# Performance work log

Hardware: AMD Instinct MI355X
Metric: run time of the kernel (lower is better)

## Reference

```python
import jax, jax.numpy as jnp
import numpy as np

B, S, H = 2, 1024, 2048
NH, NKV, HD = 16, 8, 128
GROUPS = NH // NKV
THETA = 1000000.0
SPARSITY = 0.4  # q_len > 512 -> vision_sparse_attention_sparsity_ratio
TOP_K = max(1, min(S, int(SPARSITY * S)))


def _rope(q, k, position_ids):
    # inv_freq: [HD/2]
    inv_freq = 1.0 / (THETA ** (jnp.arange(0, HD, 2, dtype=jnp.float32) / HD))
    freqs = position_ids.astype(jnp.float32)[:, :, None] * inv_freq  # [B,S,HD/2]
    emb = jnp.concatenate([freqs, freqs], axis=-1)                   # [B,S,HD]
    cos = jnp.cos(emb)[:, None].astype(q.dtype)  # [B,1,S,HD] (unsqueeze_dim=1)
    sin = jnp.sin(emb)[:, None].astype(q.dtype)
    rot = lambda x: jnp.concatenate([-x[..., HD // 2:], x[..., :HD // 2]], axis=-1)
    return q * cos + rot(q) * sin, k * cos + rot(k) * sin


def setup_inputs() -> dict:
    key = jax.random.key(0)
    ks = jax.random.split(key, 10)
    sc = 0.02
    inp = {
        'hidden_states': jax.random.normal(ks[0], (B, S, H), jnp.float32),
        'wq': jax.random.normal(ks[1], (NH * HD, H), jnp.float32) * sc,
        'bq': jax.random.normal(ks[2], (NH * HD,), jnp.float32) * sc,
        'wk': jax.random.normal(ks[3], (NKV * HD, H), jnp.float32) * sc,
        'bk': jax.random.normal(ks[4], (NKV * HD,), jnp.float32) * sc,
        'wv': jax.random.normal(ks[5], (NKV * HD, H), jnp.float32) * sc,
        'bv': jax.random.normal(ks[6], (NKV * HD,), jnp.float32) * sc,
        'wo': jax.random.normal(ks[7], (H, NH * HD), jnp.float32) * sc,
        'bo': jax.random.normal(ks[8], (H,), jnp.float32) * sc,
        'position_ids': jnp.tile(jnp.arange(S, dtype=jnp.int32)[None, :], (B, 1)),
    }
    return inp


def reference(hidden_states, wq, bq, wk, bk, wv, bv, wo, bo, position_ids):
    # QKV projections -> [B, heads, S, HD]
    q = (hidden_states @ wq.T + bq).reshape(B, S, NH, HD).transpose(0, 2, 1, 3)
    k = (hidden_states @ wk.T + bk).reshape(B, S, NKV, HD).transpose(0, 2, 1, 3)
    v = (hidden_states @ wv.T + bv).reshape(B, S, NKV, HD).transpose(0, 2, 1, 3)

    q, k = _rope(q, k, position_ids)

    # GQA: repeat_interleave KV heads along head axis
    k = jnp.repeat(k, GROUPS, axis=1)
    v = jnp.repeat(v, GROUPS, axis=1)

    scores = jnp.einsum('bhqd,bhkd->bhqk', q, k) / jnp.sqrt(jnp.float32(HD))

    # VectorizedSparseAttention: keep top-k weights per query, -inf elsewhere
    topk_vals = jax.lax.top_k(scores, TOP_K)[0]          # sorted descending
    thresh = topk_vals[..., -1:]                         # k-th largest per row
    sparse = jnp.where(scores >= thresh, scores, -jnp.inf)

    probs = jax.nn.softmax(sparse.astype(jnp.float32), axis=-1).astype(q.dtype)
    attn = jnp.einsum('bhqk,bhkd->bhqd', probs, v)       # [B,NH,S,HD]
    attn = attn.transpose(0, 2, 1, 3).reshape(B, S, NH * HD)
    return attn @ wo.T + bo
```

## Files before the change

kernel.cpp:

```cpp
#include <hip/hip_runtime.h>
#include <hip/hip_bf16.h>

constexpr int B_ = 2, S_ = 1024, H_ = 2048;
constexpr int NH_ = 16, NKV_ = 8, HD_ = 128, GROUPS_ = 2;
constexpr int TOPK_ = 409;
constexpr int QSTRIDE = NH_ * HD_;
constexpr int KSTRIDE = NKV_ * HD_;
constexpr int QB_ = 16;

typedef __attribute__((ext_vector_type(8))) short short8;
typedef __attribute__((ext_vector_type(4))) float f32x4;
typedef __attribute__((ext_vector_type(4))) unsigned u32x4;
typedef __attribute__((ext_vector_type(4))) unsigned short ush4;

__device__ inline unsigned fkey(float x) {
  unsigned u = __float_as_uint(x);
  return (u & 0x80000000u) ? ~u : (u | 0x80000000u);
}
__device__ inline unsigned short bf16_rne(float x) {
  unsigned u = __float_as_uint(x);
  unsigned r = u + 0x7FFFu + ((u >> 16) & 1u);
  return (unsigned short)(r >> 16);
}
__device__ inline float bf16_to_f(unsigned short h) {
  return __uint_as_float((unsigned)h << 16);
}
__device__ inline unsigned packsplit(float x) {
  unsigned u = __float_as_uint(x);
  unsigned r = (u + 0x7FFFu + ((u >> 16) & 1u)) & 0xFFFF0000u;
  float rem = x - __uint_as_float(r);
  unsigned v = __float_as_uint(rem);
  unsigned l = (v + 0x7FFFu + ((v >> 16) & 1u)) >> 16;
  return r | l;
}

#define PERM_HI 0x07060302u
#define PERM_LO 0x05040100u

__device__ inline void unpack8(const unsigned* p, short8& hi, short8& lo) {
  u32x4 w0 = *(const u32x4*)p;
  u32x4 w1 = *(const u32x4*)(p + 4);
  u32x4 h, l;
  h.x = __builtin_amdgcn_perm(w0.y, w0.x, PERM_HI);
  h.y = __builtin_amdgcn_perm(w0.w, w0.z, PERM_HI);
  h.z = __builtin_amdgcn_perm(w1.y, w1.x, PERM_HI);
  h.w = __builtin_amdgcn_perm(w1.w, w1.z, PERM_HI);
  l.x = __builtin_amdgcn_perm(w0.y, w0.x, PERM_LO);
  l.y = __builtin_amdgcn_perm(w0.w, w0.z, PERM_LO);
  l.z = __builtin_amdgcn_perm(w1.y, w1.x, PERM_LO);
  l.w = __builtin_amdgcn_perm(w1.w, w1.z, PERM_LO);
  hi = *(short8*)&h;
  lo = *(short8*)&l;
}
__device__ inline void unpack8r(u32x4 w0, u32x4 w1, short8& hi, short8& lo) {
  u32x4 h, l;
  h.x = __builtin_amdgcn_perm(w0.y, w0.x, PERM_HI);
  h.y = __builtin_amdgcn_perm(w0.w, w0.z, PERM_HI);
  h.z = __builtin_amdgcn_perm(w1.y, w1.x, PERM_HI);
  h.w = __builtin_amdgcn_perm(w1.w, w1.z, PERM_HI);
  l.x = __builtin_amdgcn_perm(w0.y, w0.x, PERM_LO);
  l.y = __builtin_amdgcn_perm(w0.w, w0.z, PERM_LO);
  l.z = __builtin_amdgcn_perm(w1.y, w1.x, PERM_LO);
  l.w = __builtin_amdgcn_perm(w1.w, w1.z, PERM_LO);
  hi = *(short8*)&h;
  lo = *(short8*)&l;
}

__device__ inline void wave_lds_fence() {
  asm volatile("s_waitcnt lgkmcnt(0)" ::: "memory");
}

template <int TI>
__device__ __forceinline__ void gemm_split_body(
    const float* __restrict__ A, const float* __restrict__ W,
    const float* __restrict__ bias, float* __restrict__ C, int ldc, int c0,
    int K, int m0) {
  __shared__ unsigned short Ah[2][TI * 32 * 32];
  __shared__ unsigned short Al[2][TI * 32 * 32];
  __shared__ unsigned short Wh[2][128 * 32];
  __shared__ unsigned short Wl[2][128 * 32];
  const int tid = threadIdx.x;
  const int lane = tid & 63, wid = tid >> 6;
  const int wrow = (wid >> 1) * (TI * 16), wcol = (wid & 1) * 64;
  const int fm = lane & 15, quad = lane >> 4;
  const int srow = tid >> 3;
  const int skq = (tid & 7) * 4;
  f32x4 acc[TI][4] = {};
  float4 avr[TI], wvr[4];

  auto loadAW = [&](int k0) {
#pragma unroll
    for (int r = 0; r < TI; ++r)
      avr[r] = *(const float4*)&A[(size_t)(m0 + srow + 32 * r) * K + k0 + skq];
#pragma unroll
    for (int r = 0; r < 4; ++r)
      wvr[r] = *(const float4*)&W[(size_t)(srow + 32 * r) * K + k0 + skq];
  };
  auto convWrite = [&](int buf) {
#pragma unroll
    for (int r = 0; r < TI; ++r) {
      const int row = srow + 32 * r;
      const int off =
          row * 32 + ((((skq >> 3) ^ ((row >> 1) & 3)) << 3) | (skq & 7));
      unsigned short h0 = bf16_rne(avr[r].x), h1 = bf16_rne(avr[r].y),
                     h2 = bf16_rne(avr[r].z), h3 = bf16_rne(avr[r].w);
      ush4 hv; hv.x = h0; hv.y = h1; hv.z = h2; hv.w = h3;
      ush4 lv;
      lv.x = bf16_rne(avr[r].x - bf16_to_f(h0));
      lv.y = bf16_rne(avr[r].y - bf16_to_f(h1));
      lv.z = bf16_rne(avr[r].z - bf16_to_f(h2));
      lv.w = bf16_rne(avr[r].w - bf16_to_f(h3));
      *(ush4*)&Ah[buf][off] = hv;
      *(ush4*)&Al[buf][off] = lv;
    }
#pragma unroll
    for (int r = 0; r < 4; ++r) {
      const int row = srow + 32 * r;
      const int off =
          row * 32 + ((((skq >> 3) ^ ((row >> 1) & 3)) << 3) | (skq & 7));
      unsigned short g0 = bf16_rne(wvr[r].x), g1 = bf16_rne(wvr[r].y),
                     g2 = bf16_rne(wvr[r].z), g3 = bf16_rne(wvr[r].w);
      ush4 hv; hv.x = g0; hv.y = g1; hv.z = g2; hv.w = g3;
      ush4 lv;
      lv.x = bf16_rne(wvr[r].x - bf16_to_f(g0));
      lv.y = bf16_rne(wvr[r].y - bf16_to_f(g1));
      lv.z = bf16_rne(wvr[r].z - bf16_to_f(g2));
      lv.w = bf16_rne(wvr[r].w - bf16_to_f(g3));
      *(ush4*)&Wh[buf][off] = hv;
      *(ush4*)&Wl[buf][off] = lv;
    }
  };

  loadAW(0);
  convWrite(0);
  __syncthreads();
  int cur = 0;
  for (int k0 = 0; k0 < K; k0 += 32) {
    const bool more = (k0 + 32) < K;
    if (more) loadAW(k0 + 32);
    short8 ah[TI], al[TI], bh[4], bl[4];
#pragma unroll
    for (int ti = 0; ti < TI; ++ti) {
      const int r = wrow + 16 * ti + fm;
      const int off = r * 32 + ((quad ^ ((r >> 1) & 3)) << 3);
      ah[ti] = *(const short8*)&Ah[cur][off];
      al[ti] = *(const short8*)&Al[cur][off];
    }
#pragma unroll
    for (int tj = 0; tj < 4; ++tj) {
      const int r = wcol + 16 * tj + fm;
      const int off = r * 32 + ((quad ^ ((r >> 1) & 3)) << 3);
      bh[tj] = *(const short8*)&Wh[cur][off];
      bl[tj] = *(const short8*)&Wl[cur][off];
    }
#pragma unroll
    for (int ti = 0; ti < TI; ++ti)
#pragma unroll
      for (int tj = 0; tj < 4; ++tj) {
        acc[ti][tj] = __builtin_amdgcn_mfma_f32_16x16x32_bf16(
            ah[ti], bh[tj], acc[ti][tj], 0, 0, 0);
        acc[ti][tj] = __builtin_amdgcn_mfma_f32_16x16x32_bf16(
            ah[ti], bl[tj], acc[ti][tj], 0, 0, 0);
        acc[ti][tj] = __builtin_amdgcn_mfma_f32_16x16x32_bf16(
            al[ti], bh[tj], acc[ti][tj], 0, 0, 0);
      }
    if (more) convWrite(cur ^ 1);
    __syncthreads();
    cur ^= 1;
  }
#pragma unroll
  for (int tj = 0; tj < 4; ++tj) {
    float bsv = bias[wcol + 16 * tj + fm];
#pragma unroll
    for (int ti = 0; ti < TI; ++ti) {
      int mrow = m0 + wrow + 16 * ti + quad * 4;
      int ncol = c0 + wcol + 16 * tj + fm;
#pragma unroll
      for (int reg = 0; reg < 4; ++reg)
        C[(size_t)(mrow + reg) * ldc + ncol] = acc[ti][tj][reg] + bsv;
    }
  }
}

__global__ __launch_bounds__(256) void gemm_qkv(
    const float* __restrict__ hidden, const float* __restrict__ wq,
    const float* __restrict__ bq, const float* __restrict__ wk,
    const float* __restrict__ bk, const float* __restrict__ wv,
    const float* __restrict__ bv, float* __restrict__ q, float* __restrict__ k,
    float* __restrict__ v) {
  const int n0 = blockIdx.x * 128, m0 = blockIdx.y * 128;
  const float* W;
  const float* bias;
  float* C;
  int ldc, c0;
  if (n0 < QSTRIDE) {
    W = wq + (size_t)n0 * H_; bias = bq + n0; C = q; ldc = QSTRIDE; c0 = n0;
  } else if (n0 < QSTRIDE + KSTRIDE) {
    int nn = n0 - QSTRIDE;
    W = wk + (size_t)nn * H_; bias = bk + nn; C = k; ldc = KSTRIDE; c0 = nn;
  } else {
    int nn = n0 - QSTRIDE - KSTRIDE;
    W = wv + (size_t)nn * H_; bias = bv + nn; C = v; ldc = KSTRIDE; c0 = nn;
  }
  gemm_split_body<4>(hidden, W, bias, C, ldc, c0, H_, m0);
}

template <int TI>
__global__ __launch_bounds__(256) void gemm_split_k(
    const float* __restrict__ A, const float* __restrict__ W,
    const float* __restrict__ bias, float* __restrict__ C, int N, int K) {
  const int n0 = blockIdx.x * 128, m0 = blockIdx.y * (TI * 32);
  gemm_split_body<TI>(A, W + (size_t)n0 * K, bias + n0, C, N, n0, K, m0);
}

__global__ __launch_bounds__(256) void rope_pack(float* __restrict__ qtmp,
                                                 float* __restrict__ ktmp,
                                                 float* __restrict__ vtmp,
                                                 const int* __restrict__ pos_ids) {
  const int s = blockIdx.x, b = blockIdx.y;
  const int t = threadIdx.x;
  __shared__ float fsh[64];
  if (t < 64) fsh[t] = (float)(1.0 / pow(1.0e6, (double)t / 64.0));
  __syncthreads();
  const int pos = pos_ids[b * S_ + s];
#pragma unroll
  for (int it = 0; it < 8; ++it) {
    const int p = t + 256 * it;
    const int slot = p >> 6;
    const int d = p & 63;
    float* base;
    if (slot < NH_)
      base = qtmp + (size_t)(b * S_ + s) * QSTRIDE + slot * HD_;
    else if (slot < NH_ + NKV_)
      base = ktmp + (size_t)(b * S_ + s) * KSTRIDE + (slot - NH_) * HD_;
    else
      base = vtmp + (size_t)(b * S_ + s) * KSTRIDE + (slot - NH_ - NKV_) * HD_;
    float x = base[d], y = base[d + 64];
    unsigned* up = (unsigned*)base;
    if (slot < NH_ + NKV_) {
      float ang = (float)pos * fsh[d];
      float c = cosf(ang), sn = sinf(ang);
      up[d] = packsplit(x * c - y * sn);
      up[d + 64] = packsplit(y * c + x * sn);
    } else {
      up[d] = packsplit(x);
      up[d + 64] = packsplit(y);
    }
  }
}

constexpr int SCW = 1030;

__global__ __launch_bounds__(512, 4) void attn_kernel(
    unsigned* __restrict__ qpk, const unsigned* __restrict__ kpk,
    const unsigned* __restrict__ vpk) {
  const int q0 = blockIdx.x * QB_;
  const int h = blockIdx.y, b = blockIdx.z, g = h / GROUPS_;
  const int t = threadIdx.x, lane = t & 63, wid = t >> 6;
  const int fm = lane & 15, quad = lane >> 4;

  __shared__ float sc[QB_ * SCW];
  __shared__ unsigned hist[8][256];
  __shared__ float redmx[8][QB_];
  __shared__ float Zsh[QB_];
  __shared__ unsigned prefix_sh[QB_];
  __shared__ unsigned selbin_sh[8];
  __shared__ int selkk_sh[8];
  const float scale = 0.08838834764831845f;

  short8 qh[4], ql[4];
  {
    const unsigned* qrow =
        qpk + (size_t)(b * S_ + q0 + fm) * QSTRIDE + h * HD_;
#pragma unroll
    for (int ks = 0; ks < 4; ++ks) {
      u32x4 a0 = *(const u32x4*)&qrow[ks * 32 + quad * 8];
      u32x4 a1 = *(const u32x4*)&qrow[ks * 32 + quad * 8 + 4];
      unpack8r(a0, a1, qh[ks], ql[ks]);
    }
  }

  const unsigned* kg = kpk + (size_t)(b * S_) * KSTRIDE + g * HD_;
  f32x4 mxacc = {-1e30f, -1e30f, -1e30f, -1e30f};
  for (int tile = 0; tile < 8; ++tile) {
    const unsigned* kr = kg + (size_t)(tile * 128 + wid * 16 + fm) * KSTRIDE;
    u32x4 kreg[8];
#pragma unroll
    for (int ks = 0; ks < 4; ++ks) {
      kreg[2 * ks] = *(const u32x4*)&kr[ks * 32 + quad * 8];
      kreg[2 * ks + 1] = *(const u32x4*)&kr[ks * 32 + quad * 8 + 4];
    }
    f32x4 acc = {0.f, 0.f, 0.f, 0.f};
#pragma unroll
    for (int ks = 0; ks < 4; ++ks) {
      short8 bh, bl;
      unpack8r(kreg[2 * ks], kreg[2 * ks + 1], bh, bl);
      acc = __builtin_amdgcn_mfma_f32_16x16x32_bf16(qh[ks], bh, acc, 0, 0, 0);
      acc = __builtin_amdgcn_mfma_f32_16x16x32_bf16(qh[ks], bl, acc, 0, 0, 0);
      acc = __builtin_amdgcn_mfma_f32_16x16x32_bf16(ql[ks], bh, acc, 0, 0, 0);
    }
    const int key = tile * 128 + wid * 16 + fm;
#pragma unroll
    for (int reg = 0; reg < 4; ++reg) {
      float sval = acc[reg] * scale;
      sc[(quad * 4 + reg) * SCW + key] = sval;
      mxacc[reg] = fmaxf(mxacc[reg], sval);
    }
  }
#pragma unroll
  for (int o = 1; o < 16; o <<= 1) {
    mxacc[0] = fmaxf(mxacc[0], __shfl_xor(mxacc[0], o));
    mxacc[1] = fmaxf(mxacc[1], __shfl_xor(mxacc[1], o));
    mxacc[2] = fmaxf(mxacc[2], __shfl_xor(mxacc[2], o));
    mxacc[3] = fmaxf(mxacc[3], __shfl_xor(mxacc[3], o));
  }
  if (fm == 0) {
#pragma unroll
    for (int reg = 0; reg < 4; ++reg) redmx[wid][quad * 4 + reg] = mxacc[reg];
  }
  __syncthreads();

  for (int sq = 0; sq < 2; ++sq) {
    const int qi = wid * 2 + sq;
    int kk = TOPK_;
    unsigned prefix = 0;
    for (int pass = 0; pass < 4; ++pass) {
      const int shift = 24 - 8 * pass;
      const unsigned pmask = pass ? (0xFFFFFFFFu << (shift + 8)) : 0u;
      *(u32x4*)&hist[wid][4 * lane] = (u32x4){0, 0, 0, 0};
      wave_lds_fence();
#pragma unroll 4
      for (int j = 0; j < 16; ++j) {
        unsigned u = fkey(sc[qi * SCW + lane + 64 * j]);
        if ((u & pmask) == (prefix & pmask))
          atomicAdd(&hist[wid][(u >> shift) & 255], 1u);
      }
      wave_lds_fence();
      u32x4 cw = *(const u32x4*)&hist[wid][4 * lane];
      int c0 = (int)cw.x, c1 = (int)cw.y, c2 = (int)cw.z, c3 = (int)cw.w;
      int s3 = c3, s2 = c2 + s3, s1 = c1 + s2, s0 = c0 + s1;
      int tot = s0;
      int suf = tot;
#pragma unroll
      for (int off = 1; off < 64; off <<= 1) {
        int vv = __shfl_down(suf, off);
        if (lane + off < 64) suf += vv;
      }
      int above_lanes = suf - tot;
      int i0 = s0 + above_lanes, i1 = s1 + above_lanes;
      int i2 = s2 + above_lanes, i3 = s3 + above_lanes;
      if (i3 >= kk && i3 - c3 < kk) {
        selbin_sh[wid] = (unsigned)(4 * lane + 3); selkk_sh[wid] = kk - (i3 - c3);
      }
      if (i2 >= kk && i2 - c2 < kk) {
        selbin_sh[wid] = (unsigned)(4 * lane + 2); selkk_sh[wid] = kk - (i2 - c2);
      }
      if (i1 >= kk && i1 - c1 < kk) {
        selbin_sh[wid] = (unsigned)(4 * lane + 1); selkk_sh[wid] = kk - (i1 - c1);
      }
      if (i0 >= kk && i0 - c0 < kk) {
        selbin_sh[wid] = (unsigned)(4 * lane + 0); selkk_sh[wid] = kk - (i0 - c0);
      }
      wave_lds_fence();
      prefix |= selbin_sh[wid] << shift;
      kk = selkk_sh[wid];
    }
    if (lane == 0) prefix_sh[qi] = prefix;
  }
  wave_lds_fence();

  {
    const int qi = t >> 5, li = t & 31;
    const float mx =
        fmaxf(fmaxf(fmaxf(redmx[0][qi], redmx[1][qi]),
                    fmaxf(redmx[2][qi], redmx[3][qi])),
              fmaxf(fmaxf(redmx[4][qi], redmx[5][qi]),
                    fmaxf(redmx[6][qi], redmx[7][qi])));
    const unsigned pref = prefix_sh[qi];
    unsigned* scp = (unsigned*)&sc[qi * SCW];
    float zloc = 0.f;
#pragma unroll 2
    for (int j = 0; j < 8; ++j) {
      int i4 = li * 4 + 128 * j;
      f32x4 sv = *(const f32x4*)&sc[qi * SCW + i4];
      u32x4 pk;
      float p0 = (fkey(sv.x) >= pref) ? __expf(sv.x - mx) : 0.0f;
      float p1 = (fkey(sv.y) >= pref) ? __expf(sv.y - mx) : 0.0f;
      float p2 = (fkey(sv.z) >= pref) ? __expf(sv.z - mx) : 0.0f;
      float p3 = (fkey(sv.w) >= pref) ? __expf(sv.w - mx) : 0.0f;
      zloc += p0 + p1 + p2 + p3;
      pk.x = packsplit(p0); pk.y = packsplit(p1);
      pk.z = packsplit(p2); pk.w = packsplit(p3);
      *(u32x4*)&scp[i4] = pk;
    }
#pragma unroll
    for (int off = 1; off < 32; off <<= 1) zloc += __shfl_xor(zloc, off);
    if (li == 0) Zsh[qi] = zloc;
  }
  __syncthreads();

  const unsigned* scp2 = (const unsigned*)sc;
  const unsigned* vg = vpk + (size_t)(b * S_) * KSTRIDE + g * HD_;
  f32x4 oacc = {0.f, 0.f, 0.f, 0.f};
  const int dim = wid * 16 + fm;

  auto pvstep = [&](const unsigned* w, int tile, int ksv) {
    short8 ph, pl;
    unpack8(&scp2[fm * SCW + tile * 128 + ksv * 32 + quad * 8], ph, pl);
    u32x4 hq, lq;
    hq.x = __builtin_amdgcn_perm(w[1], w[0], PERM_HI);
    hq.y = __builtin_amdgcn_perm(w[3], w[2], PERM_HI);
    hq.z = __builtin_amdgcn_perm(w[5], w[4], PERM_HI);
    hq.w = __builtin_amdgcn_perm(w[7], w[6], PERM_HI);
    lq.x = __builtin_amdgcn_perm(w[1], w[0], PERM_LO);
    lq.y = __builtin_amdgcn_perm(w[3], w[2], PERM_LO);
    lq.z = __builtin_amdgcn_perm(w[5], w[4], PERM_LO);
    lq.w = __builtin_amdgcn_perm(w[7], w[6], PERM_LO);
    short8 vh = *(short8*)&hq;
    short8 vl = *(short8*)&lq;
    oacc = __builtin_amdgcn_mfma_f32_16x16x32_bf16(ph, vh, oacc, 0, 0, 0);
    oacc = __builtin_amdgcn_mfma_f32_16x16x32_bf16(ph, vl, oacc, 0, 0, 0);
    oacc = __builtin_amdgcn_mfma_f32_16x16x32_bf16(pl, vh, oacc, 0, 0, 0);
  };

  for (int tile = 0; tile < 8; ++tile) {
    const unsigned* vb0 = vg + (size_t)(tile * 128 + quad * 8) * KSTRIDE + dim;
    unsigned va[8], vb[8];
#pragma unroll
    for (int i = 0; i < 8; ++i) va[i] = vb0[(size_t)i * KSTRIDE];
#pragma unroll
    for (int i = 0; i < 8; ++i) vb[i] = vb0[(size_t)(32 + i) * KSTRIDE];
    pvstep(va, tile, 0);
#pragma unroll
    for (int i = 0; i < 8; ++i) va[i] = vb0[(size_t)(64 + i) * KSTRIDE];
    pvstep(vb, tile, 1);
#pragma unroll
    for (int i = 0; i < 8; ++i) vb[i] = vb0[(size_t)(96 + i) * KSTRIDE];
    pvstep(va, tile, 2);
    pvstep(vb, tile, 3);
  }

#pragma unroll
  for (int reg = 0; reg < 4; ++reg) {
    const int q = quad * 4 + reg;
    const float invZ = 1.0f / Zsh[q];
    float* outp = (float*)qpk + (size_t)(b * S_ + q0 + q) * QSTRIDE + h * HD_;
    outp[dim] = oacc[reg] * invZ;
  }
}

extern "C" void kernel_launch(void* const* d_in, const int* in_sizes, int n_in,
                              void* d_out, int out_size, void* d_ws,
                              size_t ws_size, hipStream_t stream) {
  const float* hidden = (const float*)d_in[0];
  const float* wq = (const float*)d_in[1];
  const float* bq = (const float*)d_in[2];
  const float* wk = (const float*)d_in[3];
  const float* bk = (const float*)d_in[4];
  const float* wv = (const float*)d_in[5];
  const float* bv = (const float*)d_in[6];
  const float* wo = (const float*)d_in[7];
  const float* bo = (const float*)d_in[8];
  const int* pos = (const int*)d_in[9];
  float* out = (float*)d_out;

  char* ws = (char*)d_ws;
  float* qtmp = (float*)ws;
  float* ktmp = (float*)(ws + ((size_t)16 << 20));
  float* vtmp = (float*)(ws + ((size_t)24 << 20));

  dim3 blk(256);
  gemm_qkv<<<dim3(32, 16), blk, 0, stream>>>(hidden, wq, bq, wk, bk, wv, bv,
                                             qtmp, ktmp, vtmp);
  rope_pack<<<dim3(S_, B_), dim3(256), 0, stream>>>(qtmp, ktmp, vtmp, pos);
  attn_kernel<<<dim3(S_ / QB_, NH_, B_), dim3(512), 0, stream>>>(
      (unsigned*)qtmp, (const unsigned*)ktmp, (const unsigned*)vtmp);
  gemm_split_k<2><<<dim3(H_ / 128, (B_ * S_) / 64), blk, 0, stream>>>(
      qtmp, wo, bo, out, H_, H_);
}
```

Baseline: 592.7 us.

## Transpose V layout in QKV epilogue and use bitwise radix top-k select

The V projection epilogue now writes V transposed as [B,KV,HD,S], so the PV stage can load contiguous vectors per dimension instead of strided scalar loads across rows. rope_pack packs V as a flat vectorized pass. The histogram-based 4-pass radix select for the top-k threshold is replaced by a 32-step bitwise binary search held in registers, counting both query rows at once with a packed counter and wave shuffles. This removes the LDS atomics and fences but adds 32 shuffle reductions per wave.

```diff
diff --git a/kernel.cpp b/kernel.cpp
--- a/kernel.cpp
+++ b/kernel.cpp
@@ -66,11 +66,7 @@
   lo = *(short8*)&l;
 }
 
-__device__ inline void wave_lds_fence() {
-  asm volatile("s_waitcnt lgkmcnt(0)" ::: "memory");
-}
-
-template <int TI>
+template <int TI, bool VT>
 __device__ __forceinline__ void gemm_split_body(
     const float* __restrict__ A, const float* __restrict__ W,
     const float* __restrict__ bias, float* __restrict__ C, int ldc, int c0,
@@ -168,16 +164,36 @@
     __syncthreads();
     cur ^= 1;
   }
-#pragma unroll
-  for (int tj = 0; tj < 4; ++tj) {
-    float bsv = bias[wcol + 16 * tj + fm];
-#pragma unroll
-    for (int ti = 0; ti < TI; ++ti) {
-      int mrow = m0 + wrow + 16 * ti + quad * 4;
-      int ncol = c0 + wcol + 16 * tj + fm;
-#pragma unroll
-      for (int reg = 0; reg < 4; ++reg)
-        C[(size_t)(mrow + reg) * ldc + ncol] = acc[ti][tj][reg] + bsv;
+  if constexpr (VT) {
+#pragma unroll
+    for (int tj = 0; tj < 4; ++tj) {
+      float bsv = bias[wcol + 16 * tj + fm];
+#pragma unroll
+      for (int ti = 0; ti < TI; ++ti) {
+        int tok = m0 + wrow + 16 * ti + quad * 4;
+        int ncol = c0 + wcol + 16 * tj + fm;
+        int head = ncol >> 7, dim = ncol & 127;
+        int bb = tok >> 10, ss = tok & 1023;
+        float4 ov;
+        ov.x = acc[ti][tj][0] + bsv;
+        ov.y = acc[ti][tj][1] + bsv;
+        ov.z = acc[ti][tj][2] + bsv;
+        ov.w = acc[ti][tj][3] + bsv;
+        *(float4*)&C[(((size_t)(bb * NKV_ + head)) * HD_ + dim) * S_ + ss] = ov;
+      }
+    }
+  } else {
+#pragma unroll
+    for (int tj = 0; tj < 4; ++tj) {
+      float bsv = bias[wcol + 16 * tj + fm];
+#pragma unroll
+      for (int ti = 0; ti < TI; ++ti) {
+        int mrow = m0 + wrow + 16 * ti + quad * 4;
+        int ncol = c0 + wcol + 16 * tj + fm;
+#pragma unroll
+        for (int reg = 0; reg < 4; ++reg)
+          C[(size_t)(mrow + reg) * ldc + ncol] = acc[ti][tj][reg] + bsv;
+      }
     }
   }
 }
@@ -189,20 +205,18 @@
     const float* __restrict__ bv, float* __restrict__ q, float* __restrict__ k,
     float* __restrict__ v) {
   const int n0 = blockIdx.x * 128, m0 = blockIdx.y * 128;
-  const float* W;
-  const float* bias;
-  float* C;
-  int ldc, c0;
   if (n0 < QSTRIDE) {
-    W = wq + (size_t)n0 * H_; bias = bq + n0; C = q; ldc = QSTRIDE; c0 = n0;
+    gemm_split_body<4, false>(hidden, wq + (size_t)n0 * H_, bq + n0, q,
+                              QSTRIDE, n0, H_, m0);
   } else if (n0 < QSTRIDE + KSTRIDE) {
     int nn = n0 - QSTRIDE;
-    W = wk + (size_t)nn * H_; bias = bk + nn; C = k; ldc = KSTRIDE; c0 = nn;
+    gemm_split_body<4, false>(hidden, wk + (size_t)nn * H_, bk + nn, k,
+                              KSTRIDE, nn, H_, m0);
   } else {
     int nn = n0 - QSTRIDE - KSTRIDE;
-    W = wv + (size_t)nn * H_; bias = bv + nn; C = v; ldc = KSTRIDE; c0 = nn;
-  }
-  gemm_split_body<4>(hidden, W, bias, C, ldc, c0, H_, m0);
+    gemm_split_body<4, true>(hidden, wv + (size_t)nn * H_, bv + nn, v, 0, nn,
+                             H_, m0);
+  }
 }
 
 template <int TI>
@@ -210,7 +224,8 @@
     const float* __restrict__ A, const float* __restrict__ W,
     const float* __restrict__ bias, float* __restrict__ C, int N, int K) {
   const int n0 = blockIdx.x * 128, m0 = blockIdx.y * (TI * 32);
-  gemm_split_body<TI>(A, W + (size_t)n0 * K, bias + n0, C, N, n0, K, m0);
+  gemm_split_body<TI, false>(A, W + (size_t)n0 * K, bias + n0, C, N, n0, K,
+                             m0);
 }
 
 __global__ __launch_bounds__(256) void rope_pack(float* __restrict__ qtmp,
@@ -224,28 +239,29 @@
   __syncthreads();
   const int pos = pos_ids[b * S_ + s];
 #pragma unroll
-  for (int it = 0; it < 8; ++it) {
+  for (int it = 0; it < 6; ++it) {
     const int p = t + 256 * it;
     const int slot = p >> 6;
     const int d = p & 63;
-    float* base;
-    if (slot < NH_)
-      base = qtmp + (size_t)(b * S_ + s) * QSTRIDE + slot * HD_;
-    else if (slot < NH_ + NKV_)
-      base = ktmp + (size_t)(b * S_ + s) * KSTRIDE + (slot - NH_) * HD_;
-    else
-      base = vtmp + (size_t)(b * S_ + s) * KSTRIDE + (slot - NH_ - NKV_) * HD_;
+    float* base = (slot < NH_)
+                      ? qtmp + (size_t)(b * S_ + s) * QSTRIDE + slot * HD_
+                      : ktmp + (size_t)(b * S_ + s) * KSTRIDE + (slot - NH_) * HD_;
     float x = base[d], y = base[d + 64];
     unsigned* up = (unsigned*)base;
-    if (slot < NH_ + NKV_) {
-      float ang = (float)pos * fsh[d];
-      float c = cosf(ang), sn = sinf(ang);
-      up[d] = packsplit(x * c - y * sn);
-      up[d + 64] = packsplit(y * c + x * sn);
-    } else {
-      up[d] = packsplit(x);
-      up[d + 64] = packsplit(y);
-    }
+    float ang = (float)pos * fsh[d];
+    float c = cosf(ang), sn = sinf(ang);
+    up[d] = packsplit(x * c - y * sn);
+    up[d + 64] = packsplit(y * c + x * sn);
+  }
+  {
+    float* vb4 = vtmp + ((size_t)(b * S_ + s) * 1024) + t * 4;
+    float4 xv = *(float4*)vb4;
+    u32x4 pk;
+    pk.x = packsplit(xv.x);
+    pk.y = packsplit(xv.y);
+    pk.z = packsplit(xv.z);
+    pk.w = packsplit(xv.w);
+    *(u32x4*)vb4 = pk;
   }
 }
 
@@ -260,12 +276,8 @@
   const int fm = lane & 15, quad = lane >> 4;
 
   __shared__ float sc[QB_ * SCW];
-  __shared__ unsigned hist[8][256];
   __shared__ float redmx[8][QB_];
   __shared__ float Zsh[QB_];
-  __shared__ unsigned prefix_sh[QB_];
-  __shared__ unsigned selbin_sh[8];
-  __shared__ int selkk_sh[8];
   const float scale = 0.08838834764831845f;
 
   short8 qh[4], ql[4];
@@ -320,54 +332,30 @@
   }
   __syncthreads();
 
-  for (int sq = 0; sq < 2; ++sq) {
-    const int qi = wid * 2 + sq;
-    int kk = TOPK_;
-    unsigned prefix = 0;
-    for (int pass = 0; pass < 4; ++pass) {
-      const int shift = 24 - 8 * pass;
-      const unsigned pmask = pass ? (0xFFFFFFFFu << (shift + 8)) : 0u;
-      *(u32x4*)&hist[wid][4 * lane] = (u32x4){0, 0, 0, 0};
-      wave_lds_fence();
-#pragma unroll 4
-      for (int j = 0; j < 16; ++j) {
-        unsigned u = fkey(sc[qi * SCW + lane + 64 * j]);
-        if ((u & pmask) == (prefix & pmask))
-          atomicAdd(&hist[wid][(u >> shift) & 255], 1u);
-      }
-      wave_lds_fence();
-      u32x4 cw = *(const u32x4*)&hist[wid][4 * lane];
-      int c0 = (int)cw.x, c1 = (int)cw.y, c2 = (int)cw.z, c3 = (int)cw.w;
-      int s3 = c3, s2 = c2 + s3, s1 = c1 + s2, s0 = c0 + s1;
-      int tot = s0;
-      int suf = tot;
-#pragma unroll
-      for (int off = 1; off < 64; off <<= 1) {
-        int vv = __shfl_down(suf, off);
-        if (lane + off < 64) suf += vv;
-      }
-      int above_lanes = suf - tot;
-      int i0 = s0 + above_lanes, i1 = s1 + above_lanes;
-      int i2 = s2 + above_lanes, i3 = s3 + above_lanes;
-      if (i3 >= kk && i3 - c3 < kk) {
-        selbin_sh[wid] = (unsigned)(4 * lane + 3); selkk_sh[wid] = kk - (i3 - c3);
-      }
-      if (i2 >= kk && i2 - c2 < kk) {
-        selbin_sh[wid] = (unsigned)(4 * lane + 2); selkk_sh[wid] = kk - (i2 - c2);
-      }
-      if (i1 >= kk && i1 - c1 < kk) {
-        selbin_sh[wid] = (unsigned)(4 * lane + 1); selkk_sh[wid] = kk - (i1 - c1);
-      }
-      if (i0 >= kk && i0 - c0 < kk) {
-        selbin_sh[wid] = (unsigned)(4 * lane + 0); selkk_sh[wid] = kk - (i0 - c0);
-      }
-      wave_lds_fence();
-      prefix |= selbin_sh[wid] << shift;
-      kk = selkk_sh[wid];
-    }
-    if (lane == 0) prefix_sh[qi] = prefix;
-  }
-  wave_lds_fence();
+  unsigned curA = 0u, curB = 0u;
+  {
+    unsigned uvA[16], uvB[16];
+#pragma unroll
+    for (int j = 0; j < 16; ++j)
+      uvA[j] = fkey(sc[(2 * wid) * SCW + lane + 64 * j]);
+#pragma unroll
+    for (int j = 0; j < 16; ++j)
+      uvB[j] = fkey(sc[(2 * wid + 1) * SCW + lane + 64 * j]);
+    for (int bit = 31; bit >= 0; --bit) {
+      const unsigned m = 1u << bit;
+      const unsigned cA = curA | m, cB = curB | m;
+      int cnt = 0;
+#pragma unroll
+      for (int j = 0; j < 16; ++j) cnt += (uvA[j] >= cA) ? 1 : 0;
+#pragma unroll
+      for (int j = 0; j < 16; ++j) cnt += (uvB[j] >= cB) ? (1 << 16) : 0;
+#pragma unroll
+      for (int off = 1; off < 64; off <<= 1) cnt += __shfl_xor(cnt, off);
+      if ((cnt & 0xFFFF) >= TOPK_) curA = cA;
+      if ((cnt >> 16) >= TOPK_) curB = cB;
+    }
+  }
+  const unsigned pref = (lane >= 32) ? curB : curA;
 
   {
     const int qi = t >> 5, li = t & 31;
@@ -376,7 +364,6 @@
                     fmaxf(redmx[2][qi], redmx[3][qi])),
               fmaxf(fmaxf(redmx[4][qi], redmx[5][qi]),
                     fmaxf(redmx[6][qi], redmx[7][qi])));
-    const unsigned pref = prefix_sh[qi];
     unsigned* scp = (unsigned*)&sc[qi * SCW];
     float zloc = 0.f;
 #pragma unroll 2
@@ -400,44 +387,24 @@
   __syncthreads();
 
   const unsigned* scp2 = (const unsigned*)sc;
-  const unsigned* vg = vpk + (size_t)(b * S_) * KSTRIDE + g * HD_;
+  const int dim = wid * 16 + fm;
+  const unsigned* vgT =
+      vpk + ((size_t)(b * NKV_ + g) * HD_ + dim) * S_;
   f32x4 oacc = {0.f, 0.f, 0.f, 0.f};
-  const int dim = wid * 16 + fm;
-
-  auto pvstep = [&](const unsigned* w, int tile, int ksv) {
-    short8 ph, pl;
-    unpack8(&scp2[fm * SCW + tile * 128 + ksv * 32 + quad * 8], ph, pl);
-    u32x4 hq, lq;
-    hq.x = __builtin_amdgcn_perm(w[1], w[0], PERM_HI);
-    hq.y = __builtin_amdgcn_perm(w[3], w[2], PERM_HI);
-    hq.z = __builtin_amdgcn_perm(w[5], w[4], PERM_HI);
-    hq.w = __builtin_amdgcn_perm(w[7], w[6], PERM_HI);
-    lq.x = __builtin_amdgcn_perm(w[1], w[0], PERM_LO);
-    lq.y = __builtin_amdgcn_perm(w[3], w[2], PERM_LO);
-    lq.z = __builtin_amdgcn_perm(w[5], w[4], PERM_LO);
-    lq.w = __builtin_amdgcn_perm(w[7], w[6], PERM_LO);
-    short8 vh = *(short8*)&hq;
-    short8 vl = *(short8*)&lq;
-    oacc = __builtin_amdgcn_mfma_f32_16x16x32_bf16(ph, vh, oacc, 0, 0, 0);
-    oacc = __builtin_amdgcn_mfma_f32_16x16x32_bf16(ph, vl, oacc, 0, 0, 0);
-    oacc = __builtin_amdgcn_mfma_f32_16x16x32_bf16(pl, vh, oacc, 0, 0, 0);
-  };
-
   for (int tile = 0; tile < 8; ++tile) {
-    const unsigned* vb0 = vg + (size_t)(tile * 128 + quad * 8) * KSTRIDE + dim;
-    unsigned va[8], vb[8];
-#pragma unroll
-    for (int i = 0; i < 8; ++i) va[i] = vb0[(size_t)i * KSTRIDE];
-#pragma unroll
-    for (int i = 0; i < 8; ++i) vb[i] = vb0[(size_t)(32 + i) * KSTRIDE];
-    pvstep(va, tile, 0);
-#pragma unroll
-    for (int i = 0; i < 8; ++i) va[i] = vb0[(size_t)(64 + i) * KSTRIDE];
-    pvstep(vb, tile, 1);
-#pragma unroll
-    for (int i = 0; i < 8; ++i) vb[i] = vb0[(size_t)(96 + i) * KSTRIDE];
-    pvstep(va, tile, 2);
-    pvstep(vb, tile, 3);
+#pragma unroll
+    for (int ks = 0; ks < 4; ++ks) {
+      short8 ph, pl;
+      unpack8(&scp2[fm * SCW + tile * 128 + ks * 32 + quad * 8], ph, pl);
+      const unsigned* vr = vgT + tile * 128 + ks * 32 + quad * 8;
+      u32x4 b0 = *(const u32x4*)vr;
+      u32x4 b1 = *(const u32x4*)(vr + 4);
+      short8 vh, vl;
+      unpack8r(b0, b1, vh, vl);
+      oacc = __builtin_amdgcn_mfma_f32_16x16x32_bf16(ph, vh, oacc, 0, 0, 0);
+      oacc = __builtin_amdgcn_mfma_f32_16x16x32_bf16(ph, vl, oacc, 0, 0, 0);
+      oacc = __builtin_amdgcn_mfma_f32_16x16x32_bf16(pl, vh, oacc, 0, 0, 0);
+    }
   }
 
 #pragma unroll
```

New measurement: 628.5 us. +6.0%, slower.

## Replace LDS radix-histogram top-k threshold with register bitwise ballot search

Applied to the files above, without the earlier changes.

The per-row top-k threshold was found with a 4-pass 8-bit radix select using LDS atomic histograms and shuffle scans. It is now found by a 32-step bitwise binary search: each wave holds its two rows' 1024 keys in registers and counts candidates with ballot plus popcount. This removes the LDS atomics, the histogram memory and the shared prefix exchange. In exchange each wave does 32 iterations of 32 ballots, and register pressure rises by 32 values per lane.

```diff
diff --git a/kernel.cpp b/kernel.cpp
--- a/kernel.cpp
+++ b/kernel.cpp
@@ -64,10 +64,6 @@
   l.w = __builtin_amdgcn_perm(w1.w, w1.z, PERM_LO);
   hi = *(short8*)&h;
   lo = *(short8*)&l;
-}
-
-__device__ inline void wave_lds_fence() {
-  asm volatile("s_waitcnt lgkmcnt(0)" ::: "memory");
 }
 
 template <int TI>
@@ -260,12 +256,8 @@
   const int fm = lane & 15, quad = lane >> 4;
 
   __shared__ float sc[QB_ * SCW];
-  __shared__ unsigned hist[8][256];
   __shared__ float redmx[8][QB_];
   __shared__ float Zsh[QB_];
-  __shared__ unsigned prefix_sh[QB_];
-  __shared__ unsigned selbin_sh[8];
-  __shared__ int selkk_sh[8];
   const float scale = 0.08838834764831845f;
 
   short8 qh[4], ql[4];
@@ -320,54 +312,29 @@
   }
   __syncthreads();
 
-  for (int sq = 0; sq < 2; ++sq) {
-    const int qi = wid * 2 + sq;
-    int kk = TOPK_;
-    unsigned prefix = 0;
-    for (int pass = 0; pass < 4; ++pass) {
-      const int shift = 24 - 8 * pass;
-      const unsigned pmask = pass ? (0xFFFFFFFFu << (shift + 8)) : 0u;
-      *(u32x4*)&hist[wid][4 * lane] = (u32x4){0, 0, 0, 0};
-      wave_lds_fence();
-#pragma unroll 4
-      for (int j = 0; j < 16; ++j) {
-        unsigned u = fkey(sc[qi * SCW + lane + 64 * j]);
-        if ((u & pmask) == (prefix & pmask))
-          atomicAdd(&hist[wid][(u >> shift) & 255], 1u);
-      }
-      wave_lds_fence();
-      u32x4 cw = *(const u32x4*)&hist[wid][4 * lane];
-      int c0 = (int)cw.x, c1 = (int)cw.y, c2 = (int)cw.z, c3 = (int)cw.w;
-      int s3 = c3, s2 = c2 + s3, s1 = c1 + s2, s0 = c0 + s1;
-      int tot = s0;
-      int suf = tot;
-#pragma unroll
-      for (int off = 1; off < 64; off <<= 1) {
-        int vv = __shfl_down(suf, off);
-        if (lane + off < 64) suf += vv;
-      }
-      int above_lanes = suf - tot;
-      int i0 = s0 + above_lanes, i1 = s1 + above_lanes;
-      int i2 = s2 + above_lanes, i3 = s3 + above_lanes;
-      if (i3 >= kk && i3 - c3 < kk) {
-        selbin_sh[wid] = (unsigned)(4 * lane + 3); selkk_sh[wid] = kk - (i3 - c3);
-      }
-      if (i2 >= kk && i2 - c2 < kk) {
-        selbin_sh[wid] = (unsigned)(4 * lane + 2); selkk_sh[wid] = kk - (i2 - c2);
-      }
-      if (i1 >= kk && i1 - c1 < kk) {
-        selbin_sh[wid] = (unsigned)(4 * lane + 1); selkk_sh[wid] = kk - (i1 - c1);
-      }
-      if (i0 >= kk && i0 - c0 < kk) {
-        selbin_sh[wid] = (unsigned)(4 * lane + 0); selkk_sh[wid] = kk - (i0 - c0);
-      }
-      wave_lds_fence();
-      prefix |= selbin_sh[wid] << shift;
-      kk = selkk_sh[wid];
-    }
-    if (lane == 0) prefix_sh[qi] = prefix;
-  }
-  wave_lds_fence();
+  unsigned curA = 0u, curB = 0u;
+  {
+    unsigned uvA[16], uvB[16];
+#pragma unroll
+    for (int j = 0; j < 16; ++j)
+      uvA[j] = fkey(sc[(2 * wid) * SCW + lane + 64 * j]);
+#pragma unroll
+    for (int j = 0; j < 16; ++j)
+      uvB[j] = fkey(sc[(2 * wid + 1) * SCW + lane + 64 * j]);
+    for (int bit = 31; bit >= 0; --bit) {
+      const unsigned cA = curA | (1u << bit), cB = curB | (1u << bit);
+      int cntA = 0, cntB = 0;
+#pragma unroll
+      for (int j = 0; j < 16; ++j)
+        cntA += __popcll(__ballot(uvA[j] >= cA));
+#pragma unroll
+      for (int j = 0; j < 16; ++j)
+        cntB += __popcll(__ballot(uvB[j] >= cB));
+      if (cntA >= TOPK_) curA = cA;
+      if (cntB >= TOPK_) curB = cB;
+    }
+  }
+  const unsigned pref = (lane >= 32) ? curB : curA;
 
   {
     const int qi = t >> 5, li = t & 31;
@@ -376,7 +343,6 @@
                     fmaxf(redmx[2][qi], redmx[3][qi])),
               fmaxf(fmaxf(redmx[4][qi], redmx[5][qi]),
                     fmaxf(redmx[6][qi], redmx[7][qi])));
-    const unsigned pref = prefix_sh[qi];
     unsigned* scp = (unsigned*)&sc[qi * SCW];
     float zloc = 0.f;
 #pragma unroll 2
```

Result: faster. 558.4 us (-5.8%).
